# Kernel optimization log

Measured on AMD Instinct MI355X. Metric: run time of the kernel, lower is better.

## Reference

```python
import jax, jax.numpy as jnp
import numpy as np

N = 100000   # num_nodes
E = 1600000  # num_edges
D = 64       # input_dim
H = 64       # hidden_dim
G = 64       # num graphs in batch


def gcn_conv(x, row, col, ew, W, b):
    """PyG GCNConv with edge_weight and self-loops (weight 1.0).
    out = D^{-1/2} (A + I) D^{-1/2} X W + b, aggregating src->dst (row->col)."""
    h = x @ W  # [N, H]
    deg = jax.ops.segment_sum(ew, col, num_segments=N) + 1.0  # self-loop weight 1
    dinv = jnp.where(deg > 0, jax.lax.rsqrt(deg), 0.0)
    norm = dinv[row] * ew * dinv[col]                     # [E]
    agg = jax.ops.segment_sum(h[row] * norm[:, None], col, num_segments=N)
    out = agg + h * (dinv * dinv)[:, None]                # self-loop term
    return out + b


def setup_inputs() -> dict:
    key = jax.random.key(0)
    ks = jax.random.split(key, 20)
    def w(i, shape, fan_in):
        return (jax.random.uniform(ks[i], shape, jnp.float32) * 2.0 - 1.0) / np.sqrt(fan_in)
    inp = {
        "x": jax.random.normal(ks[0], (N, D), jnp.float32),
        "edge_index": jax.random.randint(ks[1], (2, E), 0, N, dtype=jnp.int64),
        "edge_attr": jax.random.uniform(ks[2], (E, 1), jnp.float32),
        "batch": jnp.sort(jax.random.randint(ks[3], (N,), 0, G, dtype=jnp.int64)),
        # GCN layers
        "W0": w(4, (D, H), D), "b0": w(5, (H,), D),
        "W1": w(6, (H, H), H), "b1": w(7, (H,), H),
        "W2": w(8, (H, H), H), "b2": w(9, (H,), H),
        "fc1_w": w(10, (H, H // 2), H), "fc1_b": w(11, (H // 2,), H),
        "fc2_w": w(12, (H // 2, 1), H // 2), "fc2_b": w(13, (1,), H // 2),
        "out_w": w(14, (1, 1), 1), "out_b": w(15, (1,), 1),
    }
    return inp


def reference(x, edge_index, edge_attr, batch, W0, b0, W1, b1, W2, b2,
              fc1_w, fc1_b, fc2_w, fc2_b, out_w, out_b):
    row, col = edge_index[0], edge_index[1]
    ew = edge_attr.reshape(-1)  # edge_attr.view(-1) used as edge_weight
    h = gcn_conv(x, row, col, ew, W0, b0)
    h = jax.nn.relu(h)  # dropout is identity in eval mode
    h = gcn_conv(h, row, col, ew, W1, b1)
    h = jax.nn.relu(h)
    h = gcn_conv(h, row, col, ew, W2, b2)  # no relu after last conv
    # global_mean_pool over batch indices
    sums = jax.ops.segment_sum(h, batch, num_segments=G)            # [G, H]
    cnts = jax.ops.segment_sum(jnp.ones((N,), h.dtype), batch, num_segments=G)
    g = sums / jnp.maximum(cnts, 1.0)[:, None]
    g = jax.nn.relu(g @ fc1_w + fc1_b)
    g = g @ fc2_w + fc2_b                  # [G, 1]
    return g @ out_w + out_b               # [G, 1]
```

## Files before the change

### kernel.cpp

```cpp
#include <hip/hip_runtime.h>
#include <hip/hip_bf16.h>

#define NN 100000
#define NE 1600000
#define DIM 64
#define NG 64

#define NBUK 391
#define EPB 4096
#define NBLK 391

typedef float fvec2 __attribute__((ext_vector_type(2)));

static __device__ __forceinline__ unsigned short bf16bits(float v) {
    __hip_bfloat16 b = __float2bfloat16(v);
    return *reinterpret_cast<unsigned short*>(&b);
}
static __device__ __forceinline__ void fp8x4(unsigned w, float& a, float& b, float& c, float& d) {
    fvec2 lo = __builtin_amdgcn_cvt_pk_f32_fp8((int)w, false);
    fvec2 hi = __builtin_amdgcn_cvt_pk_f32_fp8((int)w, true);
    a = lo[0]; b = lo[1]; c = hi[0]; d = hi[1];
}
static __device__ __forceinline__ unsigned fp8pack4(float a, float b, float c, float d) {
    int w = __builtin_amdgcn_cvt_pk_fp8_f32(a, b, 0, false);
    w = __builtin_amdgcn_cvt_pk_fp8_f32(c, d, w, true);
    return (unsigned)w;
}
static __device__ __forceinline__ unsigned csr_pack(int r, float w) {
    unsigned u = __float_as_uint(w);
    unsigned nb = ((u + 0x8000u) >> 16) & 0x7FFFu;
    return ((unsigned)r << 15) | nb;
}
static __device__ __forceinline__ float csr_w(unsigned u) {
    return __uint_as_float((u & 0x7FFFu) << 16);
}

__global__ __launch_bounds__(1024) void k_ghist2(const int* __restrict__ col,
                                                 int* __restrict__ hist2d,
                                                 int* gcnt, int E) {
    __shared__ int hist[NBUK];
    int t = threadIdx.x;
    for (int i = t; i < NBUK; i += 1024) hist[i] = 0;
    __syncthreads();
    int e0 = blockIdx.x * EPB, e1 = min(e0 + EPB, E);
    for (int e = e0 + t; e < e1; e += 1024) atomicAdd(&hist[col[e] >> 8], 1);
    __syncthreads();
    for (int i = t; i < NBUK; i += 1024) {
        int c = hist[i];
        hist2d[blockIdx.x * NBUK + i] = c;
        if (c) atomicAdd(&gcnt[i], c);
    }
}

__global__ __launch_bounds__(256) void k_gscan(const int* __restrict__ gcnt,
                                               int* __restrict__ boff,
                                               float* __restrict__ sums,
                                               float* __restrict__ cntf) {
    __shared__ int sm[256];
    int t = threadIdx.x;
    for (int i = t; i < NG * DIM; i += 256) sums[i] = 0.f;
    if (t < NG) cntf[t] = 0.f;
    int v0 = (2 * t < NBUK) ? gcnt[2 * t] : 0;
    int v1 = (2 * t + 1 < NBUK) ? gcnt[2 * t + 1] : 0;
    int s = v0 + v1;
    sm[t] = s;
    __syncthreads();
    for (int off = 1; off < 256; off <<= 1) {
        int tmp = (t >= off) ? sm[t - off] : 0;
        __syncthreads();
        sm[t] += tmp;
        __syncthreads();
    }
    int run = sm[t] - s;
    if (2 * t < NBUK) boff[2 * t] = run;
    run += v0;
    if (2 * t + 1 < NBUK) boff[2 * t + 1] = run;
    if (t == 255) boff[NBUK] = run + v1;
}

__global__ __launch_bounds__(256) void k_colscan(const int* __restrict__ hist2d,
                                                 const int* __restrict__ boff,
                                                 int* __restrict__ base2d) {
    __shared__ int sm[256];
    int b = blockIdx.x, t = threadIdx.x;
    int v0 = (2 * t < NBLK) ? hist2d[(size_t)(2 * t) * NBUK + b] : 0;
    int v1 = (2 * t + 1 < NBLK) ? hist2d[(size_t)(2 * t + 1) * NBUK + b] : 0;
    int s = v0 + v1;
    sm[t] = s;
    __syncthreads();
    for (int off = 1; off < 256; off <<= 1) {
        int tmp = (t >= off) ? sm[t - off] : 0;
        __syncthreads();
        sm[t] += tmp;
        __syncthreads();
    }
    int run = boff[b] + sm[t] - s;
    if (2 * t < NBLK) base2d[(size_t)(2 * t) * NBUK + b] = run;
    run += v0;
    if (2 * t + 1 < NBLK) base2d[(size_t)(2 * t + 1) * NBUK + b] = run;
}

__global__ __launch_bounds__(1024) void k_part1v2(const int* __restrict__ row,
                                                  const int* __restrict__ col,
                                                  const float* __restrict__ ew,
                                                  const int* __restrict__ base2d,
                                                  int2* __restrict__ binned, int E) {
    __shared__ int cur[NBUK];
    int t = threadIdx.x;
    for (int i = t; i < NBUK; i += 1024) cur[i] = base2d[(size_t)blockIdx.x * NBUK + i];
    __syncthreads();
    int e0 = blockIdx.x * EPB, e1 = min(e0 + EPB, E);
    for (int e = e0 + t; e < e1; e += 1024) {
        int c = col[e];
        int b = c >> 8, cl = c & 255;
        int p = atomicAdd(&cur[b], 1);
        binned[p] = make_int2((cl << 17) | row[e], __float_as_int(ew[e]));
    }
}

__global__ __launch_bounds__(256) void k_p2(const int2* __restrict__ binned,
                                            const int* __restrict__ boff,
                                            float* __restrict__ dinv,
                                            int* __restrict__ rowptr,
                                            unsigned* __restrict__ csr,
                                            const float* __restrict__ x,
                                            unsigned* __restrict__ xb) {
    int b = blockIdx.x, t = threadIdx.x;
    __shared__ unsigned int dsum[256];
    __shared__ int ncnt[256];
    __shared__ int sm[256];
    __shared__ float ldin[256];
    __shared__ int ncur[256];
    dsum[t] = 0;
    ncnt[t] = 0;
    __syncthreads();
    int e0 = boff[b], e1 = boff[b + 1];
    for (int e = e0 + t; e < e1; e += 256) {
        int2 v = binned[e];
        int cl = v.x >> 17;
        atomicAdd(&ncnt[cl], 1);
        unsigned int fx = (unsigned int)__float2uint_rn(__int_as_float(v.y) * 16777216.0f);
        atomicAdd(&dsum[cl], fx);
    }
    __syncthreads();
    int c = ncnt[t];
    sm[t] = c;
    __syncthreads();
    for (int off = 1; off < 256; off <<= 1) {
        int tmp = (t >= off) ? sm[t - off] : 0;
        __syncthreads();
        sm[t] += tmp;
        __syncthreads();
    }
    int node = b * 256 + t;
    float dv = rsqrtf(1.0f + (float)dsum[t] * (1.0f / 16777216.0f));
    int rp = e0 + sm[t] - c;
    ldin[t] = dv;
    ncur[t] = rp;
    if (node < NN) {
        rowptr[node] = rp;
        dinv[node] = dv;
    }
    if (b == 0 && t == 0) rowptr[NN] = NE;
    __syncthreads();
    for (int e = e0 + t; e < e1; e += 256) {
        int2 v = binned[e];
        int cl = v.x >> 17, r = v.x & 0x1FFFF;
        int p = atomicAdd(&ncur[cl], 1);
        csr[p] = csr_pack(r, __int_as_float(v.y));
    }
    int nfirst = b * 256;
    int nlast = min(nfirst + 256, NN);
    for (int idx = t; idx < (nlast - nfirst) * 16; idx += 256) {
        int nl = idx >> 4, q = idx & 15;
        float dvn = ldin[nl];
        float4 v = ((const float4*)x)[(size_t)(nfirst + nl) * 16 + q];
        xb[(size_t)(nfirst + nl) * 16 + q] =
            fp8pack4(v.x * dvn, v.y * dvn, v.z * dvn, v.w * dvn);
    }
}

__global__ __launch_bounds__(256, 7) void k_gg(const int* __restrict__ rowptr,
                                               const unsigned* __restrict__ csr,
                                               const uint2* __restrict__ hf8,
                                               const float* __restrict__ dinv,
                                               const float* __restrict__ W,
                                               const float* __restrict__ b,
                                               unsigned* __restrict__ out) {
    __shared__ float sW[64][64];
    __shared__ float sX[16][68];
    int tid = threadIdx.x;
#pragma unroll
    for (int i = 0; i < 4; ++i) {
        int q = tid + i * 256;
        ((float4*)&sW[0][0])[q] = ((const float4*)W)[q];
    }
    int node = blockIdx.x * 16 + (tid >> 4);
    int l = tid & 15;
    int g2 = l >> 3, sub = l & 7;
    float dv = dinv[node];
    float acc[8];
#pragma unroll
    for (int i = 0; i < 8; ++i) acc[i] = 0.f;
    if (g2 == 0) {
        uint2 v = hf8[(size_t)node * 8 + sub];
        fp8x4(v.x, acc[0], acc[1], acc[2], acc[3]);
        fp8x4(v.y, acc[4], acc[5], acc[6], acc[7]);
    }
    int e1 = rowptr[node + 1];
    int e = rowptr[node] + g2;
    unsigned p[4];
#pragma unroll
    for (int i = 0; i < 4; ++i) {
        p[i] = 0u;
        if (e + 2 * i < e1) p[i] = csr[e + 2 * i];
    }
    while (e < e1) {
        uint2 r[4];
#pragma unroll
        for (int i = 0; i < 4; ++i) {
            r[i] = make_uint2(0u, 0u);
            if (e + 2 * i < e1) r[i] = hf8[(size_t)(p[i] >> 15) * 8 + sub];
        }
        int en = e + 8;
        unsigned q[4];
#pragma unroll
        for (int i = 0; i < 4; ++i) {
            q[i] = 0u;
            if (en + 2 * i < e1) q[i] = csr[en + 2 * i];
        }
#pragma unroll
        for (int i = 0; i < 4; ++i) {
            float nm = csr_w(p[i]);
            float f0, f1, f2, f3, f4, f5, f6, f7;
            fp8x4(r[i].x, f0, f1, f2, f3);
            fp8x4(r[i].y, f4, f5, f6, f7);
            acc[0] = fmaf(f0, nm, acc[0]); acc[1] = fmaf(f1, nm, acc[1]);
            acc[2] = fmaf(f2, nm, acc[2]); acc[3] = fmaf(f3, nm, acc[3]);
            acc[4] = fmaf(f4, nm, acc[4]); acc[5] = fmaf(f5, nm, acc[5]);
            acc[6] = fmaf(f6, nm, acc[6]); acc[7] = fmaf(f7, nm, acc[7]);
        }
#pragma unroll
        for (int i = 0; i < 4; ++i) p[i] = q[i];
        e = en;
    }
#pragma unroll
    for (int i = 0; i < 8; ++i) acc[i] += __shfl_xor(acc[i], 8);
    if (g2 == 0) {
        int c = tid >> 4;
        *(float4*)&sX[c][sub * 8 + 0] = make_float4(acc[0] * dv, acc[1] * dv, acc[2] * dv, acc[3] * dv);
        *(float4*)&sX[c][sub * 8 + 4] = make_float4(acc[4] * dv, acc[5] * dv, acc[6] * dv, acc[7] * dv);
    }
    __syncthreads();
    int nl = tid >> 4, dg = tid & 15;
    float a0 = 0.f, a1 = 0.f, a2 = 0.f, a3 = 0.f;
#pragma unroll 4
    for (int k4 = 0; k4 < 16; ++k4) {
        float4 xr = *(const float4*)&sX[nl][k4 * 4];
        float4 w0 = *(const float4*)&sW[k4 * 4 + 0][dg * 4];
        float4 w1 = *(const float4*)&sW[k4 * 4 + 1][dg * 4];
        float4 w2 = *(const float4*)&sW[k4 * 4 + 2][dg * 4];
        float4 w3 = *(const float4*)&sW[k4 * 4 + 3][dg * 4];
        a0 = fmaf(xr.x, w0.x, a0); a1 = fmaf(xr.x, w0.y, a1);
        a2 = fmaf(xr.x, w0.z, a2); a3 = fmaf(xr.x, w0.w, a3);
        a0 = fmaf(xr.y, w1.x, a0); a1 = fmaf(xr.y, w1.y, a1);
        a2 = fmaf(xr.y, w1.z, a2); a3 = fmaf(xr.y, w1.w, a3);
        a0 = fmaf(xr.z, w2.x, a0); a1 = fmaf(xr.z, w2.y, a1);
        a2 = fmaf(xr.z, w2.z, a2); a3 = fmaf(xr.z, w2.w, a3);
        a0 = fmaf(xr.w, w3.x, a0); a1 = fmaf(xr.w, w3.y, a1);
        a2 = fmaf(xr.w, w3.z, a2); a3 = fmaf(xr.w, w3.w, a3);
    }
    float4 bv = ((const float4*)b)[dg];
    out[(size_t)(blockIdx.x * 16 + nl) * 16 + dg] =
        fp8pack4(fmaxf(a0 + bv.x, 0.f) * dv, fmaxf(a1 + bv.y, 0.f) * dv,
                 fmaxf(a2 + bv.z, 0.f) * dv, fmaxf(a3 + bv.w, 0.f) * dv);
}

__global__ __launch_bounds__(256) void k_gather7(const int* __restrict__ rowptr,
                                                 const unsigned* __restrict__ csr,
                                                 const uint2* __restrict__ hf8,
                                                 const float* __restrict__ dinv,
                                                 uint4* __restrict__ out, int n) {
    int tid = threadIdx.x;
    int node = blockIdx.x * 16 + (tid >> 4);
    if (node >= n) return;
    int l = tid & 15;
    int g2 = l >> 3, sub = l & 7;
    float dv = dinv[node];
    float acc[8];
#pragma unroll
    for (int i = 0; i < 8; ++i) acc[i] = 0.f;
    if (g2 == 0) {
        uint2 v = hf8[(size_t)node * 8 + sub];
        fp8x4(v.x, acc[0], acc[1], acc[2], acc[3]);
        fp8x4(v.y, acc[4], acc[5], acc[6], acc[7]);
    }
    int e1 = rowptr[node + 1];
    int e = rowptr[node] + g2;
    unsigned p[4];
#pragma unroll
    for (int i = 0; i < 4; ++i) {
        p[i] = 0u;
        if (e + 2 * i < e1) p[i] = csr[e + 2 * i];
    }
    while (e < e1) {
        uint2 r[4];
#pragma unroll
        for (int i = 0; i < 4; ++i) {
            r[i] = make_uint2(0u, 0u);
            if (e + 2 * i < e1) r[i] = hf8[(size_t)(p[i] >> 15) * 8 + sub];
        }
        int en = e + 8;
        unsigned q[4];
#pragma unroll
        for (int i = 0; i < 4; ++i) {
            q[i] = 0u;
            if (en + 2 * i < e1) q[i] = csr[en + 2 * i];
        }
#pragma unroll
        for (int i = 0; i < 4; ++i) {
            float nm = csr_w(p[i]);
            float f0, f1, f2, f3, f4, f5, f6, f7;
            fp8x4(r[i].x, f0, f1, f2, f3);
            fp8x4(r[i].y, f4, f5, f6, f7);
            acc[0] = fmaf(f0, nm, acc[0]); acc[1] = fmaf(f1, nm, acc[1]);
            acc[2] = fmaf(f2, nm, acc[2]); acc[3] = fmaf(f3, nm, acc[3]);
            acc[4] = fmaf(f4, nm, acc[4]); acc[5] = fmaf(f5, nm, acc[5]);
            acc[6] = fmaf(f6, nm, acc[6]); acc[7] = fmaf(f7, nm, acc[7]);
        }
#pragma unroll
        for (int i = 0; i < 4; ++i) p[i] = q[i];
        e = en;
    }
#pragma unroll
    for (int i = 0; i < 8; ++i) acc[i] += __shfl_xor(acc[i], 8);
    if (g2 == 0) {
        uint4 o;
        o.x = ((unsigned int)bf16bits(acc[1] * dv) << 16) | bf16bits(acc[0] * dv);
        o.y = ((unsigned int)bf16bits(acc[3] * dv) << 16) | bf16bits(acc[2] * dv);
        o.z = ((unsigned int)bf16bits(acc[5] * dv) << 16) | bf16bits(acc[4] * dv);
        o.w = ((unsigned int)bf16bits(acc[7] * dv) << 16) | bf16bits(acc[6] * dv);
        out[(size_t)node * 8 + sub] = o;
    }
}

static __device__ __forceinline__ void bf2x(unsigned int u, float& lo, float& hi) {
    lo = __uint_as_float(u << 16);
    hi = __uint_as_float(u & 0xFFFF0000u);
}

#define PB3 512
__global__ __launch_bounds__(256) void k_pool3(const int* __restrict__ batch,
                                               const uint4* __restrict__ h8,
                                               float* sums, float* cnt, int n) {
    __shared__ float gsum[64][65];
    __shared__ float gcl[64];
    int t = threadIdx.x;
    for (int i = t; i < 64 * 65; i += 256) (&gsum[0][0])[i] = 0.f;
    if (t < 64) gcl[t] = 0.f;
    __syncthreads();
    int base = blockIdx.x * PB3;
    int end = min(base + PB3, n);
    int g0 = batch[base];
    int cl = t >> 3, sub = t & 7;
    float acc[8];
#pragma unroll
    for (int i = 0; i < 8; ++i) acc[i] = 0.f;
    int gcur = -1, runlen = 0;
    for (int node = base + cl; node < end; node += 32) {
        int g = batch[node];
        if (g != gcur) {
            if (gcur >= 0) {
                int gl = gcur - g0;
#pragma unroll
                for (int i = 0; i < 8; ++i) atomicAdd(&gsum[gl][sub * 8 + i], acc[i]);
                if (sub == 0) atomicAdd(&gcl[gl], (float)runlen);
#pragma unroll
                for (int i = 0; i < 8; ++i) acc[i] = 0.f;
            }
            gcur = g;
            runlen = 0;
        }
        uint4 v = h8[(size_t)node * 8 + sub];
        float lo, hi;
        bf2x(v.x, lo, hi); acc[0] += lo; acc[1] += hi;
        bf2x(v.y, lo, hi); acc[2] += lo; acc[3] += hi;
        bf2x(v.z, lo, hi); acc[4] += lo; acc[5] += hi;
        bf2x(v.w, lo, hi); acc[6] += lo; acc[7] += hi;
        runlen++;
    }
    if (gcur >= 0) {
        int gl = gcur - g0;
#pragma unroll
        for (int i = 0; i < 8; ++i) atomicAdd(&gsum[gl][sub * 8 + i], acc[i]);
        if (sub == 0) atomicAdd(&gcl[gl], (float)runlen);
    }
    __syncthreads();
    int g1 = batch[end - 1];
    int ngr = g1 - g0 + 1;
    for (int idx = t; idx < ngr * 64; idx += 256) {
        int gl = idx >> 6, d = idx & 63;
        float v = gsum[gl][d];
        if (v != 0.f) atomicAdd(&sums[(g0 + gl) * DIM + d], v);
    }
    if (t < ngr) {
        float c = gcl[t];
        if (c != 0.f) atomicAdd(&cnt[g0 + t], c);
    }
}

__global__ __launch_bounds__(64) void k_head(const float* __restrict__ sums,
                                             const float* __restrict__ cnt,
                                             const float* __restrict__ W2,
                                             const float* __restrict__ b2,
                                             const float* __restrict__ fc1w,
                                             const float* __restrict__ fc1b,
                                             const float* __restrict__ fc2w,
                                             const float* __restrict__ fc2b,
                                             const float* __restrict__ ow,
                                             const float* __restrict__ ob,
                                             float* __restrict__ out) {
    int g = blockIdx.x;
    int t = threadIdx.x;
    __shared__ float gv[64];
    __shared__ float tv[64];
    float c = fmaxf(cnt[g], 1.0f);
    gv[t] = sums[g * DIM + t] / c;
    __syncthreads();
    float acc2 = b2[t];
#pragma unroll
    for (int k = 0; k < 64; ++k) acc2 = fmaf(gv[k], W2[k * 64 + t], acc2);
    tv[t] = acc2;
    __syncthreads();
    float r = 0.0f;
    if (t < 32) {
        float acc = fc1b[t];
#pragma unroll
        for (int k = 0; k < 64; ++k) acc = fmaf(tv[k], fc1w[k * 32 + t], acc);
        acc = fmaxf(acc, 0.0f);
        r = acc * fc2w[t];
    }
#pragma unroll
    for (int off = 16; off; off >>= 1) r += __shfl_down(r, off);
    if (t == 0) out[g] = (r + fc2b[0]) * ow[0] + ob[0];
}

extern "C" void kernel_launch(void* const* d_in, const int* in_sizes, int n_in,
                              void* d_out, int out_size, void* d_ws, size_t ws_size,
                              hipStream_t stream) {
    const float* x   = (const float*)d_in[0];
    const int* eidx  = (const int*)d_in[1];
    const float* ew  = (const float*)d_in[2];
    const int* batch = (const int*)d_in[3];
    const float* W0  = (const float*)d_in[4];
    const float* b0  = (const float*)d_in[5];
    const float* W1  = (const float*)d_in[6];
    const float* b1  = (const float*)d_in[7];
    const float* W2  = (const float*)d_in[8];
    const float* b2  = (const float*)d_in[9];
    const float* fc1w = (const float*)d_in[10];
    const float* fc1b = (const float*)d_in[11];
    const float* fc2w = (const float*)d_in[12];
    const float* fc2b = (const float*)d_in[13];
    const float* ow   = (const float*)d_in[14];
    const float* ob   = (const float*)d_in[15];
    float* out = (float*)d_out;

    const int* row = eidx;
    const int* col = eidx + NE;

    char* ws = (char*)d_ws;
    int2* binned           = (int2*)ws;               ws += sizeof(int2) * NE;
    unsigned* csr          = (unsigned*)ws;           ws += sizeof(unsigned) * NE;
    unsigned* Xf8          = (unsigned*)ws;           ws += sizeof(unsigned) * (size_t)NN * 16;
    unsigned* Hf8          = (unsigned*)ws;           ws += sizeof(unsigned) * (size_t)NN * 16;
    __hip_bfloat16* Hb16   = (__hip_bfloat16*)ws;     ws += sizeof(__hip_bfloat16) * (size_t)NN * DIM;
    int*   hist2d          = (int*)ws;                ws += sizeof(int) * (size_t)NBLK * NBUK;
    int*   base2d          = (int*)ws;                ws += sizeof(int) * (size_t)NBLK * NBUK;
    float* dinv            = (float*)ws;              ws += sizeof(float) * NN;
    int*   rowptr          = (int*)ws;                ws += sizeof(int) * (NN + 1);
    int*   gcnt            = (int*)ws;                ws += sizeof(int) * (NBUK + 1);
    int*   boff            = (int*)ws;                ws += sizeof(int) * (NBUK + 1);
    float* sums            = (float*)ws;              ws += sizeof(float) * NG * DIM;
    float* cntf            = (float*)ws;              ws += sizeof(float) * NG;

    hipMemsetAsync(gcnt, 0, sizeof(int) * NBUK, stream);
    k_ghist2<<<NBLK, 1024, 0, stream>>>(col, hist2d, gcnt, NE);
    k_gscan<<<1, 256, 0, stream>>>(gcnt, boff, sums, cntf);
    k_colscan<<<NBUK, 256, 0, stream>>>(hist2d, boff, base2d);
    k_part1v2<<<NBLK, 1024, 0, stream>>>(row, col, ew, base2d, binned, NE);
    k_p2<<<NBUK, 256, 0, stream>>>(binned, boff, dinv, rowptr, csr, x, Xf8);

    int gg_blocks = NN / 16;

    k_gg<<<gg_blocks, 256, 0, stream>>>(rowptr, csr, (const uint2*)Xf8, dinv, W0, b0, Hf8);
    k_gg<<<gg_blocks, 256, 0, stream>>>(rowptr, csr, (const uint2*)Hf8, dinv, W1, b1, Xf8);

    k_gather7<<<gg_blocks, 256, 0, stream>>>(rowptr, csr, (const uint2*)Xf8, dinv, (uint4*)Hb16, NN);
    k_pool3<<<(NN + PB3 - 1) / PB3, 256, 0, stream>>>(batch, (const uint4*)Hb16, sums, cntf, NN);
    k_head<<<NG, 64, 0, stream>>>(sums, cntf, W2, b2, fc1w, fc1b, fc2w, fc2b, ow, ob, out);
}
```

Measured before the change: 183.0 us.

## Fuse final-layer gather with mean-pool to skip bf16 intermediate

Merges the last aggregation kernel into the global mean-pool kernel. Each 1024-thread block now aggregates 64 nodes and accumulates the results straight into shared-memory per-graph sums, so the bf16 node-feature buffer is never written and reread. The cost is one extra block-wide barrier and more shared-memory and global atomics, since blocks now cover 64 nodes instead of 512.

After: 201.3 us. 10.0% more time.

```diff
diff --git a/kernel.cpp b/kernel.cpp
--- a/kernel.cpp
+++ b/kernel.cpp
@@ -276,136 +276,93 @@
                  fmaxf(a2 + bv.z, 0.f) * dv, fmaxf(a3 + bv.w, 0.f) * dv);
 }
 
-__global__ __launch_bounds__(256) void k_gather7(const int* __restrict__ rowptr,
-                                                 const unsigned* __restrict__ csr,
-                                                 const uint2* __restrict__ hf8,
-                                                 const float* __restrict__ dinv,
-                                                 uint4* __restrict__ out, int n) {
-    int tid = threadIdx.x;
-    int node = blockIdx.x * 16 + (tid >> 4);
-    if (node >= n) return;
-    int l = tid & 15;
-    int g2 = l >> 3, sub = l & 7;
-    float dv = dinv[node];
-    float acc[8];
-#pragma unroll
-    for (int i = 0; i < 8; ++i) acc[i] = 0.f;
-    if (g2 == 0) {
-        uint2 v = hf8[(size_t)node * 8 + sub];
-        fp8x4(v.x, acc[0], acc[1], acc[2], acc[3]);
-        fp8x4(v.y, acc[4], acc[5], acc[6], acc[7]);
-    }
-    int e1 = rowptr[node + 1];
-    int e = rowptr[node] + g2;
-    unsigned p[4];
-#pragma unroll
-    for (int i = 0; i < 4; ++i) {
-        p[i] = 0u;
-        if (e + 2 * i < e1) p[i] = csr[e + 2 * i];
-    }
-    while (e < e1) {
-        uint2 r[4];
-#pragma unroll
-        for (int i = 0; i < 4; ++i) {
-            r[i] = make_uint2(0u, 0u);
-            if (e + 2 * i < e1) r[i] = hf8[(size_t)(p[i] >> 15) * 8 + sub];
-        }
-        int en = e + 8;
-        unsigned q[4];
-#pragma unroll
-        for (int i = 0; i < 4; ++i) {
-            q[i] = 0u;
-            if (en + 2 * i < e1) q[i] = csr[en + 2 * i];
-        }
-#pragma unroll
-        for (int i = 0; i < 4; ++i) {
-            float nm = csr_w(p[i]);
-            float f0, f1, f2, f3, f4, f5, f6, f7;
-            fp8x4(r[i].x, f0, f1, f2, f3);
-            fp8x4(r[i].y, f4, f5, f6, f7);
-            acc[0] = fmaf(f0, nm, acc[0]); acc[1] = fmaf(f1, nm, acc[1]);
-            acc[2] = fmaf(f2, nm, acc[2]); acc[3] = fmaf(f3, nm, acc[3]);
-            acc[4] = fmaf(f4, nm, acc[4]); acc[5] = fmaf(f5, nm, acc[5]);
-            acc[6] = fmaf(f6, nm, acc[6]); acc[7] = fmaf(f7, nm, acc[7]);
-        }
-#pragma unroll
-        for (int i = 0; i < 4; ++i) p[i] = q[i];
-        e = en;
-    }
-#pragma unroll
-    for (int i = 0; i < 8; ++i) acc[i] += __shfl_xor(acc[i], 8);
-    if (g2 == 0) {
-        uint4 o;
-        o.x = ((unsigned int)bf16bits(acc[1] * dv) << 16) | bf16bits(acc[0] * dv);
-        o.y = ((unsigned int)bf16bits(acc[3] * dv) << 16) | bf16bits(acc[2] * dv);
-        o.z = ((unsigned int)bf16bits(acc[5] * dv) << 16) | bf16bits(acc[4] * dv);
-        o.w = ((unsigned int)bf16bits(acc[7] * dv) << 16) | bf16bits(acc[6] * dv);
-        out[(size_t)node * 8 + sub] = o;
-    }
-}
-
-static __device__ __forceinline__ void bf2x(unsigned int u, float& lo, float& hi) {
-    lo = __uint_as_float(u << 16);
-    hi = __uint_as_float(u & 0xFFFF0000u);
-}
-
-#define PB3 512
-__global__ __launch_bounds__(256) void k_pool3(const int* __restrict__ batch,
-                                               const uint4* __restrict__ h8,
-                                               float* sums, float* cnt, int n) {
+#define GPN 64
+__global__ __launch_bounds__(1024) void k_gp(const int* __restrict__ rowptr,
+                                             const unsigned* __restrict__ csr,
+                                             const uint2* __restrict__ hf8,
+                                             const float* __restrict__ dinv,
+                                             const int* __restrict__ batch,
+                                             float* sums, float* cntf, int n) {
     __shared__ float gsum[64][65];
     __shared__ float gcl[64];
     int t = threadIdx.x;
-    for (int i = t; i < 64 * 65; i += 256) (&gsum[0][0])[i] = 0.f;
+    for (int i = t; i < 64 * 65; i += 1024) (&gsum[0][0])[i] = 0.f;
     if (t < 64) gcl[t] = 0.f;
     __syncthreads();
-    int base = blockIdx.x * PB3;
-    int end = min(base + PB3, n);
+    int base = blockIdx.x * GPN;
+    int node = base + (t >> 4);
+    int l = t & 15;
+    int g2 = l >> 3, sub = l & 7;
     int g0 = batch[base];
-    int cl = t >> 3, sub = t & 7;
-    float acc[8];
-#pragma unroll
-    for (int i = 0; i < 8; ++i) acc[i] = 0.f;
-    int gcur = -1, runlen = 0;
-    for (int node = base + cl; node < end; node += 32) {
-        int g = batch[node];
-        if (g != gcur) {
-            if (gcur >= 0) {
-                int gl = gcur - g0;
-#pragma unroll
-                for (int i = 0; i < 8; ++i) atomicAdd(&gsum[gl][sub * 8 + i], acc[i]);
-                if (sub == 0) atomicAdd(&gcl[gl], (float)runlen);
-#pragma unroll
-                for (int i = 0; i < 8; ++i) acc[i] = 0.f;
+    if (node < n) {
+        float dv = dinv[node];
+        float acc[8];
+#pragma unroll
+        for (int i = 0; i < 8; ++i) acc[i] = 0.f;
+        if (g2 == 0) {
+            uint2 v = hf8[(size_t)node * 8 + sub];
+            fp8x4(v.x, acc[0], acc[1], acc[2], acc[3]);
+            fp8x4(v.y, acc[4], acc[5], acc[6], acc[7]);
+        }
+        int e1 = rowptr[node + 1];
+        int e = rowptr[node] + g2;
+        unsigned p[4];
+#pragma unroll
+        for (int i = 0; i < 4; ++i) {
+            p[i] = 0u;
+            if (e + 2 * i < e1) p[i] = csr[e + 2 * i];
+        }
+        while (e < e1) {
+            uint2 r[4];
+#pragma unroll
+            for (int i = 0; i < 4; ++i) {
+                r[i] = make_uint2(0u, 0u);
+                if (e + 2 * i < e1) r[i] = hf8[(size_t)(p[i] >> 15) * 8 + sub];
             }
-            gcur = g;
-            runlen = 0;
-        }
-        uint4 v = h8[(size_t)node * 8 + sub];
-        float lo, hi;
-        bf2x(v.x, lo, hi); acc[0] += lo; acc[1] += hi;
-        bf2x(v.y, lo, hi); acc[2] += lo; acc[3] += hi;
-        bf2x(v.z, lo, hi); acc[4] += lo; acc[5] += hi;
-        bf2x(v.w, lo, hi); acc[6] += lo; acc[7] += hi;
-        runlen++;
-    }
-    if (gcur >= 0) {
-        int gl = gcur - g0;
-#pragma unroll
-        for (int i = 0; i < 8; ++i) atomicAdd(&gsum[gl][sub * 8 + i], acc[i]);
-        if (sub == 0) atomicAdd(&gcl[gl], (float)runlen);
-    }
-    __syncthreads();
+            int en = e + 8;
+            unsigned q[4];
+#pragma unroll
+            for (int i = 0; i < 4; ++i) {
+                q[i] = 0u;
+                if (en + 2 * i < e1) q[i] = csr[en + 2 * i];
+            }
+#pragma unroll
+            for (int i = 0; i < 4; ++i) {
+                float nm = csr_w(p[i]);
+                float f0, f1, f2, f3, f4, f5, f6, f7;
+                fp8x4(r[i].x, f0, f1, f2, f3);
+                fp8x4(r[i].y, f4, f5, f6, f7);
+                acc[0] = fmaf(f0, nm, acc[0]); acc[1] = fmaf(f1, nm, acc[1]);
+                acc[2] = fmaf(f2, nm, acc[2]); acc[3] = fmaf(f3, nm, acc[3]);
+                acc[4] = fmaf(f4, nm, acc[4]); acc[5] = fmaf(f5, nm, acc[5]);
+                acc[6] = fmaf(f6, nm, acc[6]); acc[7] = fmaf(f7, nm, acc[7]);
+            }
+#pragma unroll
+            for (int i = 0; i < 4; ++i) p[i] = q[i];
+            e = en;
+        }
+#pragma unroll
+        for (int i = 0; i < 8; ++i) acc[i] += __shfl_xor(acc[i], 8);
+        if (g2 == 0) {
+            int gl = batch[node] - g0;
+            float* dst = &gsum[gl][sub * 8];
+#pragma unroll
+            for (int i = 0; i < 8; ++i) atomicAdd(dst + i, acc[i] * dv);
+            if (l == 0) atomicAdd(&gcl[gl], 1.0f);
+        }
+    }
+    __syncthreads();
+    int end = min(base + GPN, n);
     int g1 = batch[end - 1];
     int ngr = g1 - g0 + 1;
-    for (int idx = t; idx < ngr * 64; idx += 256) {
+    for (int idx = t; idx < ngr * 64; idx += 1024) {
         int gl = idx >> 6, d = idx & 63;
         float v = gsum[gl][d];
         if (v != 0.f) atomicAdd(&sums[(g0 + gl) * DIM + d], v);
     }
     if (t < ngr) {
         float c = gcl[t];
-        if (c != 0.f) atomicAdd(&cnt[g0 + t], c);
+        if (c != 0.f) atomicAdd(&cntf[g0 + t], c);
     }
 }
 
@@ -474,7 +431,6 @@
     unsigned* csr          = (unsigned*)ws;           ws += sizeof(unsigned) * NE;
     unsigned* Xf8          = (unsigned*)ws;           ws += sizeof(unsigned) * (size_t)NN * 16;
     unsigned* Hf8          = (unsigned*)ws;           ws += sizeof(unsigned) * (size_t)NN * 16;
-    __hip_bfloat16* Hb16   = (__hip_bfloat16*)ws;     ws += sizeof(__hip_bfloat16) * (size_t)NN * DIM;
     int*   hist2d          = (int*)ws;                ws += sizeof(int) * (size_t)NBLK * NBUK;
     int*   base2d          = (int*)ws;                ws += sizeof(int) * (size_t)NBLK * NBUK;
     float* dinv            = (float*)ws;              ws += sizeof(float) * NN;
@@ -492,11 +448,11 @@
     k_p2<<<NBUK, 256, 0, stream>>>(binned, boff, dinv, rowptr, csr, x, Xf8);
 
     int gg_blocks = NN / 16;
+    int gp_blocks = (NN + GPN - 1) / GPN;
 
     k_gg<<<gg_blocks, 256, 0, stream>>>(rowptr, csr, (const uint2*)Xf8, dinv, W0, b0, Hf8);
     k_gg<<<gg_blocks, 256, 0, stream>>>(rowptr, csr, (const uint2*)Hf8, dinv, W1, b1, Xf8);
 
-    k_gather7<<<gg_blocks, 256, 0, stream>>>(rowptr, csr, (const uint2*)Xf8, dinv, (uint4*)Hb16, NN);
-    k_pool3<<<(NN + PB3 - 1) / PB3, 256, 0, stream>>>(batch, (const uint4*)Hb16, sums, cntf, NN);
+    k_gp<<<gp_blocks, 1024, 0, stream>>>(rowptr, csr, (const uint2*)Xf8, dinv, batch, sums, cntf, NN);
     k_head<<<NG, 64, 0, stream>>>(sums, cntf, W2, b2, fc1w, fc1b, fc2w, fc2b, ow, ob, out);
 }
```
